# Kernel optimization log

Measured on AMD Instinct MI355X. Metric: run time of the kernel, lower is better.

The kernel has to match this reference:

```python
import jax, jax.numpy as jnp
import numpy as np
from jax import lax

K = 3
STRIDE = 2
PADDING = 1
OUTPUT_PADDING = 1


def setup_inputs() -> dict:
    key = jax.random.key(0)
    k1, k2, k3, k4 = jax.random.split(key, 4)
    B, C, H, W = 4, 64, 128, 128
    outC = 64
    g_ch = 3
    x = jax.random.normal(k1, (B, C, H, W), dtype=jnp.float32)
    guide = jax.random.normal(k2, (B, g_ch, H * STRIDE, W * STRIDE), dtype=jnp.float32)
    # kaiming-uniform-like init scale: bound = 1/sqrt(fan_in), fan_in = C*K*K
    fan_in = C * K * K
    bound = 1.0 / np.sqrt(fan_in)
    weight = jax.random.uniform(k3, (C, outC, K, K), dtype=jnp.float32, minval=-bound, maxval=bound)
    bias = jax.random.uniform(k4, (outC,), dtype=jnp.float32, minval=-bound, maxval=bound)
    return {"x": x, "guide": guide, "weight": weight, "bias": bias}


def _patches(t, pad):
    # torch.nn.functional.unfold equivalent: channel ordering (C, kh, kw)
    return lax.conv_general_dilated_patches(
        t, filter_shape=(K, K), window_strides=(1, 1), padding=[(pad, pad), (pad, pad)]
    )


def reference(x, guide, weight, bias):
    B, C, H, W = x.shape
    _, g_ch, GH, GW = guide.shape
    s, p, op = STRIDE, PADDING, OUTPUT_PADDING

    # Gaussian affinity kernel from guide patches
    gp = (K - 1) // 2
    guide_unf = _patches(guide, gp).reshape(B, g_ch, K * K, GH, GW)
    diff = guide_unf - guide_unf[:, :, K * K // 2 : K * K // 2 + 1]
    kern = jnp.exp(-0.5 * jnp.sum(diff * diff, axis=1))  # [B, K*K, GH, GW]
    kern = kern.reshape(B, 1, K, K, GH, GW)

    # depthwise transposed conv with all-ones 1x1 kernel == zero-stuffing upsample
    Ht, Wt = (H - 1) * s + 1, (W - 1) * s + 1
    temp = jnp.zeros((B, C, Ht, Wt), dtype=x.dtype).at[:, :, ::s, ::s].set(x)
    pad = (K - 1) - p
    temp = jnp.pad(temp, ((0, 0), (0, 0), (pad, pad + op), (pad, pad + op)))

    cols = _patches(temp, 0).reshape(B, C, K, K, GH, GW)
    in_mul_k = cols * kern  # [B, C, K, K, GH, GW]
    out = jnp.einsum("bcklhw,cokl->bohw", in_mul_k, weight)
    return out + bias.reshape(1, -1, 1, 1)
```

## Files before the change

kernel.cpp:

```cpp
#include <hip/hip_runtime.h>
#include <math.h>

typedef __attribute__((ext_vector_type(8))) short short8;
typedef __attribute__((ext_vector_type(4))) float float4v;

#define GH_ 256
#define GW_ 256
#define H_  128
#define W_  128
#define C_  64
#define OC_ 64
#define NB_ 4

static __device__ __forceinline__ unsigned short f2bf(float f) {
    union { float f; unsigned int u; } v; v.f = f;
    unsigned int u = v.u;
    unsigned int r = u + 0x7FFFu + ((u >> 16) & 1u);
    return (unsigned short)(r >> 16);
}

__global__ __launch_bounds__(256) void prep(const float* __restrict__ x,
                                            const float* __restrict__ w,
                                            unsigned short* __restrict__ xbf,
                                            unsigned short* __restrict__ wtb) {
    int b = blockIdx.z;
    int tid = threadIdx.x;
    if (b == 4) {
        int flat = (blockIdx.y * 2 + blockIdx.x) * 256 + tid;
        if (flat < 9 * OC_ * C_) {
            int c = flat & 63, o = (flat >> 6) & 63, t = flat >> 12;
            int kh = t / 3, kw = t - kh * 3;
            wtb[flat] = f2bf(w[((c * OC_ + o) * 3 + kh) * 3 + kw]);
        }
        return;
    }
    int half = blockIdx.x, ih = blockIdx.y;
    __shared__ float xl[C_][65];
    int iw0 = half * 64;
    for (int i = tid; i < C_ * 16; i += 256) {
        int c = i >> 4, f4 = i & 15;
        const float4* src = (const float4*)(x +
            (((size_t)(b * C_ + c) * H_) + ih) * W_ + iw0 + f4 * 4);
        float4 rd = *src;
        xl[c][f4 * 4 + 0] = rd.x;
        xl[c][f4 * 4 + 1] = rd.y;
        xl[c][f4 * 4 + 2] = rd.z;
        xl[c][f4 * 4 + 3] = rd.w;
    }
    __syncthreads();
    for (int i = tid; i < 64 * 32; i += 256) {
        int iw = i >> 5, cp = i & 31;
        unsigned int lo = f2bf(xl[2 * cp][iw]);
        unsigned int hi = f2bf(xl[2 * cp + 1][iw]);
        unsigned int* dst = (unsigned int*)(xbf +
            ((size_t)((b * H_ + ih) * W_ + iw0 + iw)) * C_);
        dst[cp] = lo | (hi << 16);
    }
}

__global__ __launch_bounds__(512, 4) void pac_main(
    const unsigned short* __restrict__ xbf,
    const float* __restrict__ guide,
    const unsigned short* __restrict__ wtb,
    const float* __restrict__ bias,
    float* __restrict__ out)
{
    const int ypair = blockIdx.x;
    const int b     = blockIdx.y;
    const int hp    = blockIdx.z;
    const int tid = threadIdx.x;
    const int ntr = 1 + hp;
    const int nslot = 3 * ntr;

    __shared__ float klds[6][2][128];

    for (int i = tid; i < nslot * 256; i += 512) {
        int px = i & 255, slot = i >> 8;
        int py = px >> 7, xp = px & 127;
        int wp, r, q;
        if (slot < ntr) { wp = 0; r = slot; q = 0; }
        else { int s = slot - ntr; wp = 1; r = s >> 1; q = s & 1; }
        int yp = ypair * 2 + py;
        int h = 2 * yp + hp, w = 2 * xp + wp;
        int rr = yp + r, cl = xp + q;
        float kv = 0.f;
        if (rr < H_ && cl < W_) {
            int hh = rr * 2, ww = cl * 2;
            const float* gb = guide + (size_t)b * 3 * GH_ * GW_;
            float s2 = 0.f;
            #pragma unroll
            for (int g = 0; g < 3; ++g) {
                float d = gb[(g * GH_ + hh) * GW_ + ww] - gb[(g * GH_ + h) * GW_ + w];
                s2 += d * d;
            }
            kv = __expf(-0.5f * s2);
        }
        klds[slot][py][xp] = kv;
    }
    __syncthreads();

    const int wave = tid >> 6, lane = tid & 63;
    const int l16 = lane & 15, qk = lane >> 4;
    const int oh  = wave & 1;
    const int py  = (wave >> 1) & 1;
    const int xh  = wave >> 2;
    const int obase = oh * 32;
    const int xpb   = xh * 64;
    const int yp = ypair * 2 + py;
    const int h  = 2 * yp + hp;

    for (int mf = 0; mf < 2; ++mf) {
        float acc0[4][4];
        float acc1[4][4];
        #pragma unroll
        for (int nf = 0; nf < 4; ++nf)
            #pragma unroll
            for (int e = 0; e < 4; ++e) { acc0[nf][e] = 0.f; acc1[nf][e] = 0.f; }

        const int o = obase + mf * 16 + l16;

        for (int r = 0; r <= hp; ++r) {
            int kh = hp ? 2 * r : 1;
            int row = yp + r; if (row > H_ - 1) row = H_ - 1;
            int s_c = r;
            int s_l = ntr + 2 * r;
            int s_r = ntr + 2 * r + 1;

            short8 af[3][2];
            #pragma unroll
            for (int kw3 = 0; kw3 < 3; ++kw3) {
                const short8* wbase = (const short8*)(wtb + (size_t)(kh * 3 + kw3) * OC_ * C_);
                af[kw3][0] = wbase[(o * C_ + qk * 8) >> 3];
                af[kw3][1] = wbase[(o * C_ + 32 + qk * 8) >> 3];
            }

            #pragma unroll
            for (int nf = 0; nf < 4; ++nf) {
                int xp = xpb + nf * 16 + l16;
                int col0 = xp;
                int col1 = xp + 1; if (col1 > W_ - 1) col1 = W_ - 1;
                const short8* xb0 = (const short8*)(xbf +
                    ((size_t)((b * H_ + row) * W_ + col0)) * C_);
                const short8* xb1 = (const short8*)(xbf +
                    ((size_t)((b * H_ + row) * W_ + col1)) * C_);
                short8 b0a = xb0[qk],     b0b = xb0[4 + qk];
                short8 b1a = xb1[qk],     b1b = xb1[4 + qk];
                float kc = klds[s_c][py][xp];
                float kl = klds[s_l][py][xp];
                float kr = klds[s_r][py][xp];
                float4v d;
                d = (float4v){0.f, 0.f, 0.f, 0.f};
                d = __builtin_amdgcn_mfma_f32_16x16x32_bf16(af[1][0], b0a, d, 0, 0, 0);
                d = __builtin_amdgcn_mfma_f32_16x16x32_bf16(af[1][1], b0b, d, 0, 0, 0);
                #pragma unroll
                for (int e = 0; e < 4; ++e) acc0[nf][e] += kc * d[e];
                d = (float4v){0.f, 0.f, 0.f, 0.f};
                d = __builtin_amdgcn_mfma_f32_16x16x32_bf16(af[0][0], b0a, d, 0, 0, 0);
                d = __builtin_amdgcn_mfma_f32_16x16x32_bf16(af[0][1], b0b, d, 0, 0, 0);
                #pragma unroll
                for (int e = 0; e < 4; ++e) acc1[nf][e] += kl * d[e];
                d = (float4v){0.f, 0.f, 0.f, 0.f};
                d = __builtin_amdgcn_mfma_f32_16x16x32_bf16(af[2][0], b1a, d, 0, 0, 0);
                d = __builtin_amdgcn_mfma_f32_16x16x32_bf16(af[2][1], b1b, d, 0, 0, 0);
                #pragma unroll
                for (int e = 0; e < 4; ++e) acc1[nf][e] += kr * d[e];
            }
        }

        float bv[4];
        #pragma unroll
        for (int e = 0; e < 4; ++e)
            bv[e] = bias[obase + mf * 16 + qk * 4 + e];

        #pragma unroll
        for (int e = 0; e < 4; ++e) {
            int oo = obase + mf * 16 + qk * 4 + e;
            float2* op = (float2*)(out + (((size_t)b * OC_ + oo) * GH_ + h) * GW_);
            #pragma unroll
            for (int nf = 0; nf < 4; ++nf) {
                int xp = xpb + nf * 16 + l16;
                float2 v;
                v.x = acc0[nf][e] + bv[e];
                v.y = acc1[nf][e] + bv[e];
                op[xp] = v;
            }
        }
    }
}

extern "C" void kernel_launch(void* const* d_in, const int* in_sizes, int n_in,
                              void* d_out, int out_size, void* d_ws, size_t ws_size,
                              hipStream_t stream) {
    const float* x     = (const float*)d_in[0];
    const float* guide = (const float*)d_in[1];
    const float* wgt   = (const float*)d_in[2];
    const float* bias  = (const float*)d_in[3];
    float* out = (float*)d_out;

    unsigned short* xbf = (unsigned short*)d_ws;
    unsigned short* wtb = xbf + (size_t)NB_ * H_ * W_ * C_;

    prep<<<dim3(2, 128, 5), 256, 0, stream>>>(x, wgt, xbf, wtb);
    pac_main<<<dim3(64, 4, 2), 512, 0, stream>>>(xbf, guide, wtb, bias, out);
}
```

Measured before the change: 119.0 us.

## Fuse x bf16 conversion into main kernel via swizzled LDS tile

Removes the separate x-to-bf16 channels-last prep pass and its global round-trip. Each block now loads the 2-3 input rows it needs straight from fp32 x, transposes and converts them in LDS, and stores them in an XOR-swizzled LDS layout for the MFMA B-operand reads. The weight conversion moves to a small separate kernel. In exchange, LDS use grows by about 56 KB per block, which may reduce occupancy, and both hp blocks of a row pair convert overlapping rows redundantly, with extra syncthreads in the load loop.

```diff
diff --git a/kernel.cpp b/kernel.cpp
--- a/kernel.cpp
+++ b/kernel.cpp
@@ -19,60 +19,68 @@
     return (unsigned short)(r >> 16);
 }
 
-__global__ __launch_bounds__(256) void prep(const float* __restrict__ x,
-                                            const float* __restrict__ w,
-                                            unsigned short* __restrict__ xbf,
-                                            unsigned short* __restrict__ wtb) {
-    int b = blockIdx.z;
-    int tid = threadIdx.x;
-    if (b == 4) {
-        int flat = (blockIdx.y * 2 + blockIdx.x) * 256 + tid;
-        if (flat < 9 * OC_ * C_) {
-            int c = flat & 63, o = (flat >> 6) & 63, t = flat >> 12;
-            int kh = t / 3, kw = t - kh * 3;
-            wtb[flat] = f2bf(w[((c * OC_ + o) * 3 + kh) * 3 + kw]);
-        }
-        return;
-    }
-    int half = blockIdx.x, ih = blockIdx.y;
-    __shared__ float xl[C_][65];
-    int iw0 = half * 64;
-    for (int i = tid; i < C_ * 16; i += 256) {
-        int c = i >> 4, f4 = i & 15;
-        const float4* src = (const float4*)(x +
-            (((size_t)(b * C_ + c) * H_) + ih) * W_ + iw0 + f4 * 4);
-        float4 rd = *src;
-        xl[c][f4 * 4 + 0] = rd.x;
-        xl[c][f4 * 4 + 1] = rd.y;
-        xl[c][f4 * 4 + 2] = rd.z;
-        xl[c][f4 * 4 + 3] = rd.w;
-    }
-    __syncthreads();
-    for (int i = tid; i < 64 * 32; i += 256) {
-        int iw = i >> 5, cp = i & 31;
-        unsigned int lo = f2bf(xl[2 * cp][iw]);
-        unsigned int hi = f2bf(xl[2 * cp + 1][iw]);
-        unsigned int* dst = (unsigned int*)(xbf +
-            ((size_t)((b * H_ + ih) * W_ + iw0 + iw)) * C_);
-        dst[cp] = lo | (hi << 16);
-    }
-}
-
-__global__ __launch_bounds__(512, 4) void pac_main(
-    const unsigned short* __restrict__ xbf,
+static __device__ __forceinline__ int swz(int byte) {
+    return byte ^ (((byte >> 7) & 7) << 4);
+}
+
+__global__ __launch_bounds__(512) void prep_w(const float* __restrict__ w,
+                                              unsigned short* __restrict__ wtb) {
+    const int t = blockIdx.x;
+    const int kh = t / 3, kw = t - kh * 3;
+    for (int i = threadIdx.x; i < OC_ * C_; i += 512) {
+        int c = i & 63, o = (i >> 6) & 63;
+        wtb[t * OC_ * C_ + i] = f2bf(w[((c * OC_ + o) * 3 + kh) * 3 + kw]);
+    }
+}
+
+__global__ __launch_bounds__(512, 4) void pac_fused(
+    const float* __restrict__ x,
     const float* __restrict__ guide,
     const unsigned short* __restrict__ wtb,
     const float* __restrict__ bias,
     float* __restrict__ out)
 {
+    __shared__ unsigned short xt[3 * 128 * 64];
+    __shared__ float xaux[64 * 33];
+
     const int ypair = blockIdx.x;
     const int b     = blockIdx.y;
     const int hp    = blockIdx.z;
-    const int tid = threadIdx.x;
+    const int tid   = threadIdx.x;
+    const int R0    = ypair * 2;
+    const int nrows = 2 + hp;
+
+    {
+        float (*xl)[33] = (float (*)[33])xaux;
+        const int c = tid >> 3, f4 = tid & 7;
+        for (int lr = 0; lr < nrows; ++lr) {
+            int srow = R0 + lr; if (srow > H_ - 1) srow = H_ - 1;
+            const float* xrow = x + (((size_t)(b * C_ + c) * H_) + srow) * W_;
+            for (int qtr = 0; qtr < 4; ++qtr) {
+                const int iw0 = qtr * 32;
+                float4 rd = *(const float4*)(xrow + iw0 + f4 * 4);
+                xl[c][f4 * 4 + 0] = rd.x;
+                xl[c][f4 * 4 + 1] = rd.y;
+                xl[c][f4 * 4 + 2] = rd.z;
+                xl[c][f4 * 4 + 3] = rd.w;
+                __syncthreads();
+                #pragma unroll
+                for (int j = 0; j < 2; ++j) {
+                    int jj = tid + j * 512;
+                    int cl = jj >> 5, cp = jj & 31;
+                    unsigned int lo = f2bf(xl[2 * cp][cl]);
+                    unsigned int hi = f2bf(xl[2 * cp + 1][cl]);
+                    int lin = ((lr * 128 + iw0 + cl) << 7) + cp * 4;
+                    *(unsigned int*)((char*)xt + swz(lin)) = lo | (hi << 16);
+                }
+                __syncthreads();
+            }
+        }
+    }
+
     const int ntr = 1 + hp;
     const int nslot = 3 * ntr;
-
-    __shared__ float klds[6][2][128];
+    float (*klds)[2][128] = (float (*)[2][128])xaux;
 
     for (int i = tid; i < nslot * 256; i += 512) {
         int px = i & 255, slot = i >> 8;
@@ -80,7 +88,7 @@
         int wp, r, q;
         if (slot < ntr) { wp = 0; r = slot; q = 0; }
         else { int s = slot - ntr; wp = 1; r = s >> 1; q = s & 1; }
-        int yp = ypair * 2 + py;
+        int yp = R0 + py;
         int h = 2 * yp + hp, w = 2 * xp + wp;
         int rr = yp + r, cl = xp + q;
         float kv = 0.f;
@@ -106,7 +114,7 @@
     const int xh  = wave >> 2;
     const int obase = oh * 32;
     const int xpb   = xh * 64;
-    const int yp = ypair * 2 + py;
+    const int yp = R0 + py;
     const int h  = 2 * yp + hp;
 
     for (int mf = 0; mf < 2; ++mf) {
@@ -121,7 +129,8 @@
 
         for (int r = 0; r <= hp; ++r) {
             int kh = hp ? 2 * r : 1;
-            int row = yp + r; if (row > H_ - 1) row = H_ - 1;
+            int rowc = yp + r; if (rowc > H_ - 1) rowc = H_ - 1;
+            int lr0 = rowc - R0;
             int s_c = r;
             int s_l = ntr + 2 * r;
             int s_r = ntr + 2 * r + 1;
@@ -137,14 +146,13 @@
             #pragma unroll
             for (int nf = 0; nf < 4; ++nf) {
                 int xp = xpb + nf * 16 + l16;
-                int col0 = xp;
                 int col1 = xp + 1; if (col1 > W_ - 1) col1 = W_ - 1;
-                const short8* xb0 = (const short8*)(xbf +
-                    ((size_t)((b * H_ + row) * W_ + col0)) * C_);
-                const short8* xb1 = (const short8*)(xbf +
-                    ((size_t)((b * H_ + row) * W_ + col1)) * C_);
-                short8 b0a = xb0[qk],     b0b = xb0[4 + qk];
-                short8 b1a = xb1[qk],     b1b = xb1[4 + qk];
+                int base0 = ((lr0 * 128 + xp)   << 7) + qk * 16;
+                int base1 = ((lr0 * 128 + col1) << 7) + qk * 16;
+                short8 b0a = *(const short8*)((const char*)xt + swz(base0));
+                short8 b0b = *(const short8*)((const char*)xt + swz(base0 + 64));
+                short8 b1a = *(const short8*)((const char*)xt + swz(base1));
+                short8 b1b = *(const short8*)((const char*)xt + swz(base1 + 64));
                 float kc = klds[s_c][py][xp];
                 float kl = klds[s_l][py][xp];
                 float kr = klds[s_r][py][xp];
@@ -197,9 +205,8 @@
     const float* bias  = (const float*)d_in[3];
     float* out = (float*)d_out;
 
-    unsigned short* xbf = (unsigned short*)d_ws;
-    unsigned short* wtb = xbf + (size_t)NB_ * H_ * W_ * C_;
-
-    prep<<<dim3(2, 128, 5), 256, 0, stream>>>(x, wgt, xbf, wtb);
-    pac_main<<<dim3(64, 4, 2), 512, 0, stream>>>(xbf, guide, wtb, bias, out);
-}
+    unsigned short* wtb = (unsigned short*)d_ws;
+
+    prep_w<<<dim3(9), 512, 0, stream>>>(wgt, wtb);
+    pac_fused<<<dim3(64, 4, 2), 512, 0, stream>>>(x, guide, wtb, bias, out);
+}
```

Result: faster. 106.2 us (-10.8%).
